# Kernel optimization log

Hardware: AMD Instinct MI355X
Metric: run time of the kernel (lower is better)

Reference implementation:

```python
import jax, jax.numpy as jnp
import numpy as np

N_NODES = 100000

def _gcn_norm(edge_index, num_nodes):
    # add self loops, compute symmetric normalization D^-1/2 (A+I) D^-1/2
    loops = jnp.arange(num_nodes, dtype=edge_index.dtype)
    row = jnp.concatenate([edge_index[0], loops])
    col = jnp.concatenate([edge_index[1], loops])
    ones = jnp.ones(row.shape[0], dtype=jnp.float32)
    deg = jax.ops.segment_sum(ones, row, num_segments=num_nodes)
    dinv = jnp.where(deg > 0, jax.lax.rsqrt(deg), 0.0)
    norm = dinv[row] * dinv[col]  # [E+N]
    return row, col, norm

def _gcn_conv(x, W, b, row, col, norm, num_nodes):
    h = x @ W                      # [N, out]
    msg = h[col] * norm[:, None]   # gather + scale, [E+N, out]
    out = jax.ops.segment_sum(msg, row, num_segments=num_nodes)
    return out + b

def setup_inputs() -> dict:
    key = jax.random.key(0)
    k1, k2, k3, k4 = jax.random.split(key, 4)
    F_IN, HID, CLS = 128, 128, 40
    E = 1_600_000
    x = jax.random.normal(k1, (N_NODES, F_IN), dtype=jnp.float32)
    edge_index = jax.random.randint(k2, (2, E), 0, N_NODES, dtype=jnp.int64)
    W1 = jax.random.normal(k3, (F_IN, HID), dtype=jnp.float32) / np.sqrt(F_IN)
    b1 = jnp.zeros((HID,), dtype=jnp.float32)
    W2 = jax.random.normal(k4, (HID, CLS), dtype=jnp.float32) / np.sqrt(HID)
    b2 = jnp.zeros((CLS,), dtype=jnp.float32)
    return {"x": x, "edge_index": edge_index, "W1": W1, "b1": b1, "W2": W2, "b2": b2}

def reference(x, edge_index, W1, b1, W2, b2):
    num_nodes = x.shape[0]
    row, col, norm = _gcn_norm(edge_index, num_nodes)
    h = _gcn_conv(x, W1, b1, row, col, norm, num_nodes)
    h = jax.nn.relu(h)
    h = _gcn_conv(h, W2, b2, row, col, norm, num_nodes)
    return jax.nn.log_softmax(h, axis=1)
```

## Files before the change

kernel.cpp:

```cpp
#include <hip/hip_runtime.h>
#include <hip/hip_bf16.h>
#include <math.h>


#define TILE_A 8192
#define RB 98
#define CAP 2048

typedef __attribute__((ext_vector_type(8))) short bf16x8;
typedef __attribute__((ext_vector_type(4))) float f32x4;
typedef __attribute__((ext_vector_type(2))) float f32x2;
typedef __attribute__((ext_vector_type(4))) unsigned int u32x4;

struct f8 { float v[8]; };

__device__ inline f8 unpack8(uint4 u) {
    f8 r;
    r.v[0] = __uint_as_float(u.x << 16);
    r.v[1] = __uint_as_float(u.x & 0xffff0000u);
    r.v[2] = __uint_as_float(u.y << 16);
    r.v[3] = __uint_as_float(u.y & 0xffff0000u);
    r.v[4] = __uint_as_float(u.z << 16);
    r.v[5] = __uint_as_float(u.z & 0xffff0000u);
    r.v[6] = __uint_as_float(u.w << 16);
    r.v[7] = __uint_as_float(u.w & 0xffff0000u);
    return r;
}

__device__ inline f8 unpack8f8(unsigned long long v) {
    f8 r;
#if __has_builtin(__builtin_amdgcn_cvt_pk_f32_fp8)
    int lo = (int)(unsigned)(v & 0xffffffffULL);
    int hi = (int)(unsigned)(v >> 32);
    f32x2 p0 = __builtin_amdgcn_cvt_pk_f32_fp8(lo, false);
    f32x2 p1 = __builtin_amdgcn_cvt_pk_f32_fp8(lo, true);
    f32x2 p2 = __builtin_amdgcn_cvt_pk_f32_fp8(hi, false);
    f32x2 p3 = __builtin_amdgcn_cvt_pk_f32_fp8(hi, true);
    r.v[0] = p0[0]; r.v[1] = p0[1]; r.v[2] = p1[0]; r.v[3] = p1[1];
    r.v[4] = p2[0]; r.v[5] = p2[1]; r.v[6] = p3[0]; r.v[7] = p3[1];
#else
#pragma unroll
    for (int k = 0; k < 8; ++k) {
        unsigned b = (unsigned)((v >> (8 * k)) & 0xffULL);
        unsigned em = b & 0x7f;
        unsigned bits = (em ? ((em << 20) + 0x3C000000u) : 0u) | ((b >> 7) << 31);
        r.v[k] = __uint_as_float(bits);
    }
#endif
    return r;
}

__device__ inline unsigned char fp8_of(float f) {
#if __has_builtin(__builtin_amdgcn_cvt_pk_fp8_f32)
    int p = __builtin_amdgcn_cvt_pk_fp8_f32(f, f, 0, false);
    return (unsigned char)(p & 0xff);
#else
    unsigned s = __float_as_uint(f) >> 31;
    float af = fabsf(f);
    if (af < 0.015625f) return (unsigned char)(s << 7);
    if (af > 448.f) af = 448.f;
    unsigned u = __float_as_uint(af);
    unsigned mant = (u >> 20) & 0x7;
    unsigned rest = u & 0xfffff;
    unsigned em = (((u >> 23) - 120) << 3) | mant;
    if (rest > 0x80000 || (rest == 0x80000 && (mant & 1))) em += 1;
    if (em > 0x7e) em = 0x7e;
    return (unsigned char)((s << 7) | em);
#endif
}

__device__ inline unsigned pack2(float a, float b) {
    __hip_bfloat16 ha = __float2bfloat16(a);
    __hip_bfloat16 hb = __float2bfloat16(b);
    unsigned short sa = *(unsigned short*)&ha;
    unsigned short sb = *(unsigned short*)&hb;
    return (unsigned)sa | ((unsigned)sb << 16);
}

__device__ inline short bfs(float f) {
    __hip_bfloat16 h = __float2bfloat16(f);
    return *(short*)&h;
}

__device__ inline bf16x8 to8(float4 p, float4 q) {
    bf16x8 v;
    v[0] = bfs(p.x); v[1] = bfs(p.y); v[2] = bfs(p.z); v[3] = bfs(p.w);
    v[4] = bfs(q.x); v[5] = bfs(q.y); v[6] = bfs(q.z); v[7] = bfs(q.w);
    return v;
}

__device__ inline int ecol_of(long long v) { return (int)(unsigned)(v & 0xffffffffLL); }
__device__ inline float ew_of(long long v) { return __int_as_float((int)(v >> 32)); }

__global__ __launch_bounds__(256) void k_wt(const float* __restrict__ W1,
                                            const float* __restrict__ W2,
                                            short* __restrict__ Wt1,
                                            short* __restrict__ Wt2,
                                            int* __restrict__ bktcnt) {
    int idx = blockIdx.x * 256 + threadIdx.x;
    if (idx < 16384) {
        int k = idx >> 7, f = idx & 127;
        Wt1[f * 128 + k] = bfs(W1[k * 128 + f]);
    } else if (idx < 16384 + 6144) {
        int j = idx - 16384;
        int f = j >> 7, k = j & 127;
        Wt2[j] = (f < 40) ? bfs(W2[k * 40 + f]) : (short)0;
    } else if (idx < 16384 + 6144 + 1024) {
        bktcnt[idx - 16384 - 6144] = 0;
    }
}

__global__ __launch_bounds__(1024) void k_binA(const int* __restrict__ ei,
                                               int* __restrict__ bktcnt,
                                               int2* __restrict__ brec, int E) {
    __shared__ int h[1024];
    __shared__ int cur[1024];
    int t = threadIdx.x;
    h[t] = 0;
    __syncthreads();
    int base = blockIdx.x * TILE_A;
    int lim = min(base + TILE_A, E);
    for (int i = base + t; i < lim; i += 1024) atomicAdd(&h[ei[i] / RB], 1);
    __syncthreads();
    cur[t] = h[t] ? atomicAdd(&bktcnt[t], h[t]) : 0;
    __syncthreads();
    for (int i = base + t; i < lim; i += 1024) {
        int r = ei[i];
        int b = r / RB;
        int pos = atomicAdd(&cur[b], 1);
        if (pos < CAP) brec[(size_t)b * CAP + pos] = make_int2(r, ei[E + i]);
    }
}

__global__ __launch_bounds__(256) void k_cnt(const int2* __restrict__ brec,
                                             const int* __restrict__ bktcnt,
                                             int2* __restrict__ rbe,
                                             float* __restrict__ dinv, int N) {
    __shared__ int h[RB];
    __shared__ int l[256];
    int k = blockIdx.x;
    int t = threadIdx.x;
    if (t < RB) h[t] = 0;
    __syncthreads();
    int s = k * CAP;
    int e = s + min(bktcnt[k], CAP);
    int r0 = k * RB;
    for (int i = s + t; i < e; i += 256) atomicAdd(&h[brec[i].x - r0], 1);
    __syncthreads();
    int v = (t < RB) ? h[t] : 0;
    l[t] = v;
    __syncthreads();
#pragma unroll
    for (int o = 1; o < 256; o <<= 1) {
        int u = (t >= o) ? l[t - o] : 0;
        __syncthreads();
        l[t] += u;
        __syncthreads();
    }
    if (t < RB && r0 + t < N) {
        int beg = s + (l[t] - v);
        rbe[r0 + t] = make_int2(beg, beg + v);
        dinv[r0 + t] = rsqrtf((float)(v + 1));
    }
}

__global__ __launch_bounds__(256) void k_csr3(const int2* __restrict__ brec,
                                              const int* __restrict__ bktcnt,
                                              const int2* __restrict__ rbe,
                                              const float* __restrict__ dinv,
                                              long long* __restrict__ erec, int N) {
    __shared__ int cur[RB];
    int k = blockIdx.x;
    int t = threadIdx.x;
    int r0 = k * RB;
    if (t < RB) cur[t] = (r0 + t < N) ? rbe[r0 + t].x : 0;
    __syncthreads();
    int s = k * CAP;
    int e = s + min(bktcnt[k], CAP);
    for (int i = s + t; i < e; i += 256) {
        int2 rc = brec[i];
        int pos = atomicAdd(&cur[rc.x - r0], 1);
        float w = dinv[rc.x] * dinv[rc.y];
        long long rec = (long long)((unsigned long long)(unsigned)__float_as_int(w) << 32) |
                        (unsigned long long)(unsigned)rc.y;
        erec[pos] = rec;
    }
}

__global__ __launch_bounds__(256) void k_gemm1m(const float* __restrict__ x,
                                                const short* __restrict__ Wt,
                                                unsigned char* __restrict__ Tf8, int N) {
    int t = threadIdx.x;
    int wid = t >> 6, l = t & 63;
    int r = l & 15;
    int ko = (l >> 4) * 8;
    long long nb = (long long)blockIdx.x * 128 + wid * 32;

    bf16x8 a[2][4];
#pragma unroll
    for (int g = 0; g < 2; ++g) {
        long long n = nb + g * 16 + r;
        if (n >= N) n = N - 1;
        const float* xr = x + n * 128;
#pragma unroll
        for (int kc = 0; kc < 4; ++kc) {
            float4 p = *(const float4*)(xr + kc * 32 + ko);
            float4 q = *(const float4*)(xr + kc * 32 + ko + 4);
            a[g][kc] = to8(p, q);
        }
    }

    f32x4 acc[2][8];
#pragma unroll
    for (int g = 0; g < 2; ++g)
#pragma unroll
        for (int ft = 0; ft < 8; ++ft) acc[g][ft] = (f32x4){0.f, 0.f, 0.f, 0.f};

#pragma unroll
    for (int ft = 0; ft < 8; ++ft) {
        const short* wp = Wt + (ft * 16 + r) * 128 + ko;
#pragma unroll
        for (int kc = 0; kc < 4; ++kc) {
            bf16x8 b = *(const bf16x8*)(wp + kc * 32);
            acc[0][ft] = __builtin_amdgcn_mfma_f32_16x16x32_bf16(a[0][kc], b, acc[0][ft], 0, 0, 0);
            acc[1][ft] = __builtin_amdgcn_mfma_f32_16x16x32_bf16(a[1][kc], b, acc[1][ft], 0, 0, 0);
        }
    }

    int row0 = (l >> 4) * 4;
#pragma unroll
    for (int g = 0; g < 2; ++g) {
#pragma unroll
        for (int i = 0; i < 4; ++i) {
            long long n = nb + g * 16 + row0 + i;
            if (n < N) {
                unsigned char* orow = Tf8 + n * 128;
#pragma unroll
                for (int ft = 0; ft < 8; ++ft) orow[ft * 16 + r] = fp8_of(acc[g][ft][i]);
            }
        }
    }
}

__global__ __launch_bounds__(256) void k_gemm2m(const short* __restrict__ Ub,
                                                const short* __restrict__ Wt2,
                                                short* __restrict__ H2a,
                                                short* __restrict__ H2c, int N) {
    int t = threadIdx.x;
    int wid = t >> 6, l = t & 63;
    int r = l & 15;
    int ko = (l >> 4) * 8;
    long long nb = (long long)blockIdx.x * 128 + wid * 32;

    bf16x8 a[2][4];
#pragma unroll
    for (int g = 0; g < 2; ++g) {
        long long n = nb + g * 16 + r;
        if (n >= N) n = N - 1;
        const short* ur = Ub + n * 128;
#pragma unroll
        for (int kc = 0; kc < 4; ++kc)
            a[g][kc] = *(const bf16x8*)(ur + kc * 32 + ko);
    }

    f32x4 acc[2][3];
#pragma unroll
    for (int g = 0; g < 2; ++g)
#pragma unroll
        for (int ft = 0; ft < 3; ++ft) acc[g][ft] = (f32x4){0.f, 0.f, 0.f, 0.f};

#pragma unroll
    for (int ft = 0; ft < 3; ++ft) {
        const short* wp = Wt2 + (ft * 16 + r) * 128 + ko;
#pragma unroll
        for (int kc = 0; kc < 4; ++kc) {
            bf16x8 b = *(const bf16x8*)(wp + kc * 32);
            acc[0][ft] = __builtin_amdgcn_mfma_f32_16x16x32_bf16(a[0][kc], b, acc[0][ft], 0, 0, 0);
            acc[1][ft] = __builtin_amdgcn_mfma_f32_16x16x32_bf16(a[1][kc], b, acc[1][ft], 0, 0, 0);
        }
    }

    int row0 = (l >> 4) * 4;
#pragma unroll
    for (int g = 0; g < 2; ++g) {
#pragma unroll
        for (int i = 0; i < 4; ++i) {
            long long n = nb + g * 16 + row0 + i;
            if (n < N) {
#pragma unroll
                for (int ft = 0; ft < 3; ++ft) {
                    int f = ft * 16 + r;
                    if (f < 32) H2a[n * 32 + f] = bfs(acc[g][ft][i]);
                    else if (f < 40) H2c[n * 8 + (f - 32)] = bfs(acc[g][ft][i]);
                }
            }
        }
    }
}

__global__ __launch_bounds__(256) void k_pull1(const unsigned long long* __restrict__ T8,
                                               const float* __restrict__ dinv,
                                               const int2* __restrict__ rbe,
                                               const long long* __restrict__ erec,
                                               const float* __restrict__ b,
                                               uint4* __restrict__ Ub, int N) {
    int tid = blockIdx.x * 256 + threadIdx.x;
    int n = tid >> 4;
    if (n >= N) return;
    int q = tid & 15;

    float dn = dinv[n];
    float ss = dn * dn;
    f8 s8 = unpack8f8(T8[(size_t)n * 16 + q]);
    float acc[8];
#pragma unroll
    for (int j = 0; j < 8; ++j) acc[j] = s8.v[j] * ss;

    int2 be = rbe[n];
    int i = be.x, end = be.y;
    for (; i + 7 < end; i += 8) {
        long long e0 = __builtin_nontemporal_load(erec + i);
        long long e1 = __builtin_nontemporal_load(erec + i + 1);
        long long e2 = __builtin_nontemporal_load(erec + i + 2);
        long long e3 = __builtin_nontemporal_load(erec + i + 3);
        long long e4 = __builtin_nontemporal_load(erec + i + 4);
        long long e5 = __builtin_nontemporal_load(erec + i + 5);
        long long e6 = __builtin_nontemporal_load(erec + i + 6);
        long long e7 = __builtin_nontemporal_load(erec + i + 7);
        unsigned long long g0 = T8[(size_t)ecol_of(e0) * 16 + q];
        unsigned long long g1 = T8[(size_t)ecol_of(e1) * 16 + q];
        unsigned long long g2 = T8[(size_t)ecol_of(e2) * 16 + q];
        unsigned long long g3 = T8[(size_t)ecol_of(e3) * 16 + q];
        unsigned long long g4 = T8[(size_t)ecol_of(e4) * 16 + q];
        unsigned long long g5 = T8[(size_t)ecol_of(e5) * 16 + q];
        unsigned long long g6 = T8[(size_t)ecol_of(e6) * 16 + q];
        unsigned long long g7 = T8[(size_t)ecol_of(e7) * 16 + q];
        f8 a0 = unpack8f8(g0);
        f8 a1 = unpack8f8(g1);
        f8 a2 = unpack8f8(g2);
        f8 a3 = unpack8f8(g3);
        f8 a4 = unpack8f8(g4);
        f8 a5 = unpack8f8(g5);
        f8 a6 = unpack8f8(g6);
        f8 a7 = unpack8f8(g7);
        float w0 = ew_of(e0), w1 = ew_of(e1), w2 = ew_of(e2), w3 = ew_of(e3);
        float w4 = ew_of(e4), w5 = ew_of(e5), w6 = ew_of(e6), w7 = ew_of(e7);
#pragma unroll
        for (int j = 0; j < 8; ++j) acc[j] = fmaf(w0, a0.v[j], acc[j]);
#pragma unroll
        for (int j = 0; j < 8; ++j) acc[j] = fmaf(w1, a1.v[j], acc[j]);
#pragma unroll
        for (int j = 0; j < 8; ++j) acc[j] = fmaf(w2, a2.v[j], acc[j]);
#pragma unroll
        for (int j = 0; j < 8; ++j) acc[j] = fmaf(w3, a3.v[j], acc[j]);
#pragma unroll
        for (int j = 0; j < 8; ++j) acc[j] = fmaf(w4, a4.v[j], acc[j]);
#pragma unroll
        for (int j = 0; j < 8; ++j) acc[j] = fmaf(w5, a5.v[j], acc[j]);
#pragma unroll
        for (int j = 0; j < 8; ++j) acc[j] = fmaf(w6, a6.v[j], acc[j]);
#pragma unroll
        for (int j = 0; j < 8; ++j) acc[j] = fmaf(w7, a7.v[j], acc[j]);
    }
    for (; i + 3 < end; i += 4) {
        long long e0 = __builtin_nontemporal_load(erec + i);
        long long e1 = __builtin_nontemporal_load(erec + i + 1);
        long long e2 = __builtin_nontemporal_load(erec + i + 2);
        long long e3 = __builtin_nontemporal_load(erec + i + 3);
        unsigned long long g0 = T8[(size_t)ecol_of(e0) * 16 + q];
        unsigned long long g1 = T8[(size_t)ecol_of(e1) * 16 + q];
        unsigned long long g2 = T8[(size_t)ecol_of(e2) * 16 + q];
        unsigned long long g3 = T8[(size_t)ecol_of(e3) * 16 + q];
        f8 a0 = unpack8f8(g0);
        f8 a1 = unpack8f8(g1);
        f8 a2 = unpack8f8(g2);
        f8 a3 = unpack8f8(g3);
        float w0 = ew_of(e0), w1 = ew_of(e1), w2 = ew_of(e2), w3 = ew_of(e3);
#pragma unroll
        for (int j = 0; j < 8; ++j) acc[j] = fmaf(w0, a0.v[j], acc[j]);
#pragma unroll
        for (int j = 0; j < 8; ++j) acc[j] = fmaf(w1, a1.v[j], acc[j]);
#pragma unroll
        for (int j = 0; j < 8; ++j) acc[j] = fmaf(w2, a2.v[j], acc[j]);
#pragma unroll
        for (int j = 0; j < 8; ++j) acc[j] = fmaf(w3, a3.v[j], acc[j]);
    }
    for (; i < end; ++i) {
        long long e0 = __builtin_nontemporal_load(erec + i);
        float w0 = ew_of(e0);
        f8 a0 = unpack8f8(T8[(size_t)ecol_of(e0) * 16 + q]);
#pragma unroll
        for (int j = 0; j < 8; ++j) acc[j] = fmaf(w0, a0.v[j], acc[j]);
    }

    float4 b0 = ((const float4*)b)[q * 2];
    float4 b1v = ((const float4*)b)[q * 2 + 1];
    acc[0] = fmaxf(acc[0] + b0.x, 0.f);
    acc[1] = fmaxf(acc[1] + b0.y, 0.f);
    acc[2] = fmaxf(acc[2] + b0.z, 0.f);
    acc[3] = fmaxf(acc[3] + b0.w, 0.f);
    acc[4] = fmaxf(acc[4] + b1v.x, 0.f);
    acc[5] = fmaxf(acc[5] + b1v.y, 0.f);
    acc[6] = fmaxf(acc[6] + b1v.z, 0.f);
    acc[7] = fmaxf(acc[7] + b1v.w, 0.f);

    uint4 o;
    o.x = pack2(acc[0], acc[1]);
    o.y = pack2(acc[2], acc[3]);
    o.z = pack2(acc[4], acc[5]);
    o.w = pack2(acc[6], acc[7]);
    Ub[(size_t)n * 16 + q] = o;
}

__global__ __launch_bounds__(256) void k_pull2(const uint4* __restrict__ H2a4,
                                               const uint4* __restrict__ H2c4,
                                               const float* __restrict__ dinv,
                                               const int2* __restrict__ rbe,
                                               const long long* __restrict__ erec,
                                               const float* __restrict__ b2,
                                               float* __restrict__ out, int N) {
    int tid = blockIdx.x * 256 + threadIdx.x;
    int n = tid >> 3;
    if (n >= N) return;
    int q = tid & 7;
    bool act = q < 5;
    bool ina = q < 4;
    const uint4* bp = ina ? (H2a4 + q) : H2c4;
    size_t stride = ina ? 4 : 1;

    float dn = dinv[n];
    float ss = dn * dn;
    float acc[8];
#pragma unroll
    for (int j = 0; j < 8; ++j) acc[j] = 0.f;
    if (act) {
        f8 s8 = unpack8(bp[(size_t)n * stride]);
#pragma unroll
        for (int j = 0; j < 8; ++j) acc[j] = s8.v[j] * ss;
    }
    int2 be = rbe[n];
    int i = be.x, end = be.y;
    for (; i + 3 < end; i += 4) {
        long long e0 = __builtin_nontemporal_load(erec + i);
        long long e1 = __builtin_nontemporal_load(erec + i + 1);
        long long e2 = __builtin_nontemporal_load(erec + i + 2);
        long long e3 = __builtin_nontemporal_load(erec + i + 3);
        uint4 g0 = bp[(size_t)ecol_of(e0) * stride];
        uint4 g1 = bp[(size_t)ecol_of(e1) * stride];
        uint4 g2 = bp[(size_t)ecol_of(e2) * stride];
        uint4 g3 = bp[(size_t)ecol_of(e3) * stride];
        if (act) {
            float w0 = ew_of(e0), w1 = ew_of(e1), w2 = ew_of(e2), w3 = ew_of(e3);
            f8 a0 = unpack8(g0);
            f8 a1 = unpack8(g1);
            f8 a2 = unpack8(g2);
            f8 a3 = unpack8(g3);
#pragma unroll
            for (int j = 0; j < 8; ++j) acc[j] = fmaf(w0, a0.v[j], acc[j]);
#pragma unroll
            for (int j = 0; j < 8; ++j) acc[j] = fmaf(w1, a1.v[j], acc[j]);
#pragma unroll
            for (int j = 0; j < 8; ++j) acc[j] = fmaf(w2, a2.v[j], acc[j]);
#pragma unroll
            for (int j = 0; j < 8; ++j) acc[j] = fmaf(w3, a3.v[j], acc[j]);
        }
    }
    for (; i < end; ++i) {
        long long e0 = erec[i];
        if (act) {
            float w0 = ew_of(e0);
            f8 a0 = unpack8(bp[(size_t)ecol_of(e0) * stride]);
#pragma unroll
            for (int j = 0; j < 8; ++j) acc[j] = fmaf(w0, a0.v[j], acc[j]);
        }
    }
    if (act) {
        float4 b0 = ((const float4*)b2)[q * 2];
        float4 b1v = ((const float4*)b2)[q * 2 + 1];
        acc[0] += b0.x; acc[1] += b0.y; acc[2] += b0.z; acc[3] += b0.w;
        acc[4] += b1v.x; acc[5] += b1v.y; acc[6] += b1v.z; acc[7] += b1v.w;
    }
    float m = -INFINITY;
    if (act) {
#pragma unroll
        for (int j = 0; j < 8; ++j) m = fmaxf(m, acc[j]);
    }
#pragma unroll
    for (int o = 4; o > 0; o >>= 1) m = fmaxf(m, __shfl_xor(m, o, 8));
    float e = 0.f;
    if (act) {
#pragma unroll
        for (int j = 0; j < 8; ++j) e += expf(acc[j] - m);
    }
#pragma unroll
    for (int o = 4; o > 0; o >>= 1) e += __shfl_xor(e, o, 8);
    float lg = m + logf(e);
    if (act) {
        float4* o4 = (float4*)out;
        o4[(size_t)n * 10 + q * 2] =
            make_float4(acc[0] - lg, acc[1] - lg, acc[2] - lg, acc[3] - lg);
        o4[(size_t)n * 10 + q * 2 + 1] =
            make_float4(acc[4] - lg, acc[5] - lg, acc[6] - lg, acc[7] - lg);
    }
}

extern "C" void kernel_launch(void* const* d_in, const int* in_sizes, int n_in,
                              void* d_out, int out_size, void* d_ws, size_t ws_size,
                              hipStream_t stream) {
    const float* x  = (const float*)d_in[0];
    const int*   ei = (const int*)d_in[1];
    const float* W1 = (const float*)d_in[2];
    const float* b1 = (const float*)d_in[3];
    const float* W2 = (const float*)d_in[4];
    const float* b2 = (const float*)d_in[5];
    float* out = (float*)d_out;

    const int N = in_sizes[0] / 128;
    const int E = in_sizes[1] / 2;
    const int nbkt = (N + RB - 1) / RB;

    char* ws = (char*)d_ws;
    float* dinv    = (float*)(ws);
    int2*  rbe     = (int2*)(ws + (512 << 10));
    int*   bktcnt  = (int*)(ws + (1536 << 10));
    short* Wt1     = (short*)(ws + (1600 << 10));
    short* Wt2     = (short*)(ws + (1700 << 10));
    long long* erec = (long long*)(ws + (3 << 20));
    int2*  brec    = (int2*)(ws + (21 << 20));
    short* H2a     = (short*)(ws + (38 << 20));
    short* H2c     = (short*)(ws + (45 << 20));
    unsigned char* Tf8 = (unsigned char*)(ws + (47 << 20));
    unsigned* Ub   = (unsigned*)(ws + (60 << 20));

    int na = (E + TILE_A - 1) / TILE_A;
    int ng = (N + 127) / 128;

    k_wt<<<92, 256, 0, stream>>>(W1, W2, Wt1, Wt2, bktcnt);
    k_binA<<<na, 1024, 0, stream>>>(ei, bktcnt, brec, E);
    k_cnt<<<nbkt, 256, 0, stream>>>(brec, bktcnt, rbe, dinv, N);
    k_csr3<<<nbkt, 256, 0, stream>>>(brec, bktcnt, rbe, dinv, erec, N);

    k_gemm1m<<<ng, 256, 0, stream>>>(x, Wt1, Tf8, N);
    k_pull1<<<((long long)N * 16 + 255) / 256, 256, 0, stream>>>(
        (const unsigned long long*)Tf8, dinv, rbe, erec, b1, (uint4*)Ub, N);
    k_gemm2m<<<ng, 256, 0, stream>>>((const short*)Ub, Wt2, H2a, H2c, N);
    k_pull2<<<((long long)N * 8 + 255) / 256, 256, 0, stream>>>(
        (const uint4*)H2a, (const uint4*)H2c, dinv, rbe, erec, b2, out, N);
}
```

Measured before the change: 177.7 us.

## Store 4-byte column indices, compute edge weights on the fly, split layer-2 pull

Replaces the 8-byte packed (weight, column) edge records with 4-byte column indices and recomputes each edge weight as dinv[n]*dinv[col] inside the pull kernels. This halves edge-stream traffic and lets the old count and CSR-fill kernels merge into one. Layer-2 features are stored in two 20-column halves, pulled by two kernel passes that write unnormalized output, and a separate log-softmax kernel then rereads and rewrites the output. The extra dinv gathers, the added launches and the second pass over the edge list and output are the costs taken on in exchange.

```diff
diff --git a/kernel.cpp b/kernel.cpp
--- a/kernel.cpp
+++ b/kernel.cpp
@@ -10,9 +10,9 @@
 typedef __attribute__((ext_vector_type(8))) short bf16x8;
 typedef __attribute__((ext_vector_type(4))) float f32x4;
 typedef __attribute__((ext_vector_type(2))) float f32x2;
-typedef __attribute__((ext_vector_type(4))) unsigned int u32x4;
 
 struct f8 { float v[8]; };
+struct f4s { float v[4]; };
 
 __device__ inline f8 unpack8(uint4 u) {
     f8 r;
@@ -24,6 +24,16 @@
     r.v[5] = __uint_as_float(u.z & 0xffff0000u);
     r.v[6] = __uint_as_float(u.w << 16);
     r.v[7] = __uint_as_float(u.w & 0xffff0000u);
+    return r;
+}
+
+__device__ inline f4s unpack4(unsigned long long v) {
+    f4s r;
+    unsigned lo = (unsigned)v, hi = (unsigned)(v >> 32);
+    r.v[0] = __uint_as_float(lo << 16);
+    r.v[1] = __uint_as_float(lo & 0xffff0000u);
+    r.v[2] = __uint_as_float(hi << 16);
+    r.v[3] = __uint_as_float(hi & 0xffff0000u);
     return r;
 }
 
@@ -89,9 +99,6 @@
     return v;
 }
 
-__device__ inline int ecol_of(long long v) { return (int)(unsigned)(v & 0xffffffffLL); }
-__device__ inline float ew_of(long long v) { return __int_as_float((int)(v >> 32)); }
-
 __global__ __launch_bounds__(256) void k_wt(const float* __restrict__ W1,
                                             const float* __restrict__ W2,
                                             short* __restrict__ Wt1,
@@ -132,12 +139,14 @@
     }
 }
 
-__global__ __launch_bounds__(256) void k_cnt(const int2* __restrict__ brec,
+__global__ __launch_bounds__(256) void k_csr(const int2* __restrict__ brec,
                                              const int* __restrict__ bktcnt,
                                              int2* __restrict__ rbe,
-                                             float* __restrict__ dinv, int N) {
+                                             float* __restrict__ dinv,
+                                             int* __restrict__ ecol, int N) {
     __shared__ int h[RB];
     __shared__ int l[256];
+    __shared__ int cur[RB];
     int k = blockIdx.x;
     int t = threadIdx.x;
     if (t < RB) h[t] = 0;
@@ -157,33 +166,19 @@
         l[t] += u;
         __syncthreads();
     }
-    if (t < RB && r0 + t < N) {
+    if (t < RB) {
         int beg = s + (l[t] - v);
-        rbe[r0 + t] = make_int2(beg, beg + v);
-        dinv[r0 + t] = rsqrtf((float)(v + 1));
-    }
-}
-
-__global__ __launch_bounds__(256) void k_csr3(const int2* __restrict__ brec,
-                                              const int* __restrict__ bktcnt,
-                                              const int2* __restrict__ rbe,
-                                              const float* __restrict__ dinv,
-                                              long long* __restrict__ erec, int N) {
-    __shared__ int cur[RB];
-    int k = blockIdx.x;
-    int t = threadIdx.x;
-    int r0 = k * RB;
-    if (t < RB) cur[t] = (r0 + t < N) ? rbe[r0 + t].x : 0;
-    __syncthreads();
-    int s = k * CAP;
-    int e = s + min(bktcnt[k], CAP);
+        cur[t] = beg;
+        if (r0 + t < N) {
+            rbe[r0 + t] = make_int2(beg, beg + v);
+            dinv[r0 + t] = rsqrtf((float)(v + 1));
+        }
+    }
+    __syncthreads();
     for (int i = s + t; i < e; i += 256) {
         int2 rc = brec[i];
         int pos = atomicAdd(&cur[rc.x - r0], 1);
-        float w = dinv[rc.x] * dinv[rc.y];
-        long long rec = (long long)((unsigned long long)(unsigned)__float_as_int(w) << 32) |
-                        (unsigned long long)(unsigned)rc.y;
-        erec[pos] = rec;
+        ecol[pos] = rc.y;
     }
 }
 
@@ -244,8 +239,8 @@
 
 __global__ __launch_bounds__(256) void k_gemm2m(const short* __restrict__ Ub,
                                                 const short* __restrict__ Wt2,
-                                                short* __restrict__ H2a,
-                                                short* __restrict__ H2c, int N) {
+                                                short* __restrict__ H2p0,
+                                                short* __restrict__ H2p1, int N) {
     int t = threadIdx.x;
     int wid = t >> 6, l = t & 63;
     int r = l & 15;
@@ -290,8 +285,8 @@
 #pragma unroll
                 for (int ft = 0; ft < 3; ++ft) {
                     int f = ft * 16 + r;
-                    if (f < 32) H2a[n * 32 + f] = bfs(acc[g][ft][i]);
-                    else if (f < 40) H2c[n * 8 + (f - 32)] = bfs(acc[g][ft][i]);
+                    if (f < 20) H2p0[n * 20 + f] = bfs(acc[g][ft][i]);
+                    else if (f < 40) H2p1[n * 20 + (f - 20)] = bfs(acc[g][ft][i]);
                 }
             }
         }
@@ -301,7 +296,7 @@
 __global__ __launch_bounds__(256) void k_pull1(const unsigned long long* __restrict__ T8,
                                                const float* __restrict__ dinv,
                                                const int2* __restrict__ rbe,
-                                               const long long* __restrict__ erec,
+                                               const int* __restrict__ ecol,
                                                const float* __restrict__ b,
                                                uint4* __restrict__ Ub, int N) {
     int tid = blockIdx.x * 256 + threadIdx.x;
@@ -319,22 +314,26 @@
     int2 be = rbe[n];
     int i = be.x, end = be.y;
     for (; i + 7 < end; i += 8) {
-        long long e0 = __builtin_nontemporal_load(erec + i);
-        long long e1 = __builtin_nontemporal_load(erec + i + 1);
-        long long e2 = __builtin_nontemporal_load(erec + i + 2);
-        long long e3 = __builtin_nontemporal_load(erec + i + 3);
-        long long e4 = __builtin_nontemporal_load(erec + i + 4);
-        long long e5 = __builtin_nontemporal_load(erec + i + 5);
-        long long e6 = __builtin_nontemporal_load(erec + i + 6);
-        long long e7 = __builtin_nontemporal_load(erec + i + 7);
-        unsigned long long g0 = T8[(size_t)ecol_of(e0) * 16 + q];
-        unsigned long long g1 = T8[(size_t)ecol_of(e1) * 16 + q];
-        unsigned long long g2 = T8[(size_t)ecol_of(e2) * 16 + q];
-        unsigned long long g3 = T8[(size_t)ecol_of(e3) * 16 + q];
-        unsigned long long g4 = T8[(size_t)ecol_of(e4) * 16 + q];
-        unsigned long long g5 = T8[(size_t)ecol_of(e5) * 16 + q];
-        unsigned long long g6 = T8[(size_t)ecol_of(e6) * 16 + q];
-        unsigned long long g7 = T8[(size_t)ecol_of(e7) * 16 + q];
+        int c0 = __builtin_nontemporal_load(ecol + i);
+        int c1 = __builtin_nontemporal_load(ecol + i + 1);
+        int c2 = __builtin_nontemporal_load(ecol + i + 2);
+        int c3 = __builtin_nontemporal_load(ecol + i + 3);
+        int c4 = __builtin_nontemporal_load(ecol + i + 4);
+        int c5 = __builtin_nontemporal_load(ecol + i + 5);
+        int c6 = __builtin_nontemporal_load(ecol + i + 6);
+        int c7 = __builtin_nontemporal_load(ecol + i + 7);
+        unsigned long long g0 = T8[(size_t)c0 * 16 + q];
+        unsigned long long g1 = T8[(size_t)c1 * 16 + q];
+        unsigned long long g2 = T8[(size_t)c2 * 16 + q];
+        unsigned long long g3 = T8[(size_t)c3 * 16 + q];
+        unsigned long long g4 = T8[(size_t)c4 * 16 + q];
+        unsigned long long g5 = T8[(size_t)c5 * 16 + q];
+        unsigned long long g6 = T8[(size_t)c6 * 16 + q];
+        unsigned long long g7 = T8[(size_t)c7 * 16 + q];
+        float w0 = dn * dinv[c0], w1 = dn * dinv[c1];
+        float w2 = dn * dinv[c2], w3 = dn * dinv[c3];
+        float w4 = dn * dinv[c4], w5 = dn * dinv[c5];
+        float w6 = dn * dinv[c6], w7 = dn * dinv[c7];
         f8 a0 = unpack8f8(g0);
         f8 a1 = unpack8f8(g1);
         f8 a2 = unpack8f8(g2);
@@ -343,8 +342,6 @@
         f8 a5 = unpack8f8(g5);
         f8 a6 = unpack8f8(g6);
         f8 a7 = unpack8f8(g7);
-        float w0 = ew_of(e0), w1 = ew_of(e1), w2 = ew_of(e2), w3 = ew_of(e3);
-        float w4 = ew_of(e4), w5 = ew_of(e5), w6 = ew_of(e6), w7 = ew_of(e7);
 #pragma unroll
         for (int j = 0; j < 8; ++j) acc[j] = fmaf(w0, a0.v[j], acc[j]);
 #pragma unroll
@@ -363,19 +360,20 @@
         for (int j = 0; j < 8; ++j) acc[j] = fmaf(w7, a7.v[j], acc[j]);
     }
     for (; i + 3 < end; i += 4) {
-        long long e0 = __builtin_nontemporal_load(erec + i);
-        long long e1 = __builtin_nontemporal_load(erec + i + 1);
-        long long e2 = __builtin_nontemporal_load(erec + i + 2);
-        long long e3 = __builtin_nontemporal_load(erec + i + 3);
-        unsigned long long g0 = T8[(size_t)ecol_of(e0) * 16 + q];
-        unsigned long long g1 = T8[(size_t)ecol_of(e1) * 16 + q];
-        unsigned long long g2 = T8[(size_t)ecol_of(e2) * 16 + q];
-        unsigned long long g3 = T8[(size_t)ecol_of(e3) * 16 + q];
+        int c0 = __builtin_nontemporal_load(ecol + i);
+        int c1 = __builtin_nontemporal_load(ecol + i + 1);
+        int c2 = __builtin_nontemporal_load(ecol + i + 2);
+        int c3 = __builtin_nontemporal_load(ecol + i + 3);
+        unsigned long long g0 = T8[(size_t)c0 * 16 + q];
+        unsigned long long g1 = T8[(size_t)c1 * 16 + q];
+        unsigned long long g2 = T8[(size_t)c2 * 16 + q];
+        unsigned long long g3 = T8[(size_t)c3 * 16 + q];
+        float w0 = dn * dinv[c0], w1 = dn * dinv[c1];
+        float w2 = dn * dinv[c2], w3 = dn * dinv[c3];
         f8 a0 = unpack8f8(g0);
         f8 a1 = unpack8f8(g1);
         f8 a2 = unpack8f8(g2);
         f8 a3 = unpack8f8(g3);
-        float w0 = ew_of(e0), w1 = ew_of(e1), w2 = ew_of(e2), w3 = ew_of(e3);
 #pragma unroll
         for (int j = 0; j < 8; ++j) acc[j] = fmaf(w0, a0.v[j], acc[j]);
 #pragma unroll
@@ -386,9 +384,9 @@
         for (int j = 0; j < 8; ++j) acc[j] = fmaf(w3, a3.v[j], acc[j]);
     }
     for (; i < end; ++i) {
-        long long e0 = __builtin_nontemporal_load(erec + i);
-        float w0 = ew_of(e0);
-        f8 a0 = unpack8f8(T8[(size_t)ecol_of(e0) * 16 + q]);
+        int c0 = __builtin_nontemporal_load(ecol + i);
+        float w0 = dn * dinv[c0];
+        f8 a0 = unpack8f8(T8[(size_t)c0 * 16 + q]);
 #pragma unroll
         for (int j = 0; j < 8; ++j) acc[j] = fmaf(w0, a0.v[j], acc[j]);
     }
@@ -412,95 +410,103 @@
     Ub[(size_t)n * 16 + q] = o;
 }
 
-__global__ __launch_bounds__(256) void k_pull2(const uint4* __restrict__ H2a4,
-                                               const uint4* __restrict__ H2c4,
-                                               const float* __restrict__ dinv,
-                                               const int2* __restrict__ rbe,
-                                               const long long* __restrict__ erec,
-                                               const float* __restrict__ b2,
-                                               float* __restrict__ out, int N) {
+__global__ __launch_bounds__(256) void k_pull2h(const unsigned long long* __restrict__ H2p,
+                                                const float* __restrict__ dinv,
+                                                const int2* __restrict__ rbe,
+                                                const int* __restrict__ ecol,
+                                                const float* __restrict__ b2,
+                                                float* __restrict__ out, int N, int hf) {
     int tid = blockIdx.x * 256 + threadIdx.x;
     int n = tid >> 3;
     if (n >= N) return;
     int q = tid & 7;
     bool act = q < 5;
-    bool ina = q < 4;
-    const uint4* bp = ina ? (H2a4 + q) : H2c4;
-    size_t stride = ina ? 4 : 1;
 
     float dn = dinv[n];
     float ss = dn * dn;
-    float acc[8];
-#pragma unroll
-    for (int j = 0; j < 8; ++j) acc[j] = 0.f;
+    float acc[4] = {0.f, 0.f, 0.f, 0.f};
     if (act) {
-        f8 s8 = unpack8(bp[(size_t)n * stride]);
-#pragma unroll
-        for (int j = 0; j < 8; ++j) acc[j] = s8.v[j] * ss;
+        f4s s4 = unpack4(H2p[(size_t)n * 5 + q]);
+#pragma unroll
+        for (int j = 0; j < 4; ++j) acc[j] = s4.v[j] * ss;
     }
     int2 be = rbe[n];
     int i = be.x, end = be.y;
     for (; i + 3 < end; i += 4) {
-        long long e0 = __builtin_nontemporal_load(erec + i);
-        long long e1 = __builtin_nontemporal_load(erec + i + 1);
-        long long e2 = __builtin_nontemporal_load(erec + i + 2);
-        long long e3 = __builtin_nontemporal_load(erec + i + 3);
-        uint4 g0 = bp[(size_t)ecol_of(e0) * stride];
-        uint4 g1 = bp[(size_t)ecol_of(e1) * stride];
-        uint4 g2 = bp[(size_t)ecol_of(e2) * stride];
-        uint4 g3 = bp[(size_t)ecol_of(e3) * stride];
+        int c0 = __builtin_nontemporal_load(ecol + i);
+        int c1 = __builtin_nontemporal_load(ecol + i + 1);
+        int c2 = __builtin_nontemporal_load(ecol + i + 2);
+        int c3 = __builtin_nontemporal_load(ecol + i + 3);
         if (act) {
-            float w0 = ew_of(e0), w1 = ew_of(e1), w2 = ew_of(e2), w3 = ew_of(e3);
-            f8 a0 = unpack8(g0);
-            f8 a1 = unpack8(g1);
-            f8 a2 = unpack8(g2);
-            f8 a3 = unpack8(g3);
-#pragma unroll
-            for (int j = 0; j < 8; ++j) acc[j] = fmaf(w0, a0.v[j], acc[j]);
-#pragma unroll
-            for (int j = 0; j < 8; ++j) acc[j] = fmaf(w1, a1.v[j], acc[j]);
-#pragma unroll
-            for (int j = 0; j < 8; ++j) acc[j] = fmaf(w2, a2.v[j], acc[j]);
-#pragma unroll
-            for (int j = 0; j < 8; ++j) acc[j] = fmaf(w3, a3.v[j], acc[j]);
+            float w0 = dn * dinv[c0], w1 = dn * dinv[c1];
+            float w2 = dn * dinv[c2], w3 = dn * dinv[c3];
+            f4s a0 = unpack4(H2p[(size_t)c0 * 5 + q]);
+            f4s a1 = unpack4(H2p[(size_t)c1 * 5 + q]);
+            f4s a2 = unpack4(H2p[(size_t)c2 * 5 + q]);
+            f4s a3 = unpack4(H2p[(size_t)c3 * 5 + q]);
+#pragma unroll
+            for (int j = 0; j < 4; ++j) acc[j] = fmaf(w0, a0.v[j], acc[j]);
+#pragma unroll
+            for (int j = 0; j < 4; ++j) acc[j] = fmaf(w1, a1.v[j], acc[j]);
+#pragma unroll
+            for (int j = 0; j < 4; ++j) acc[j] = fmaf(w2, a2.v[j], acc[j]);
+#pragma unroll
+            for (int j = 0; j < 4; ++j) acc[j] = fmaf(w3, a3.v[j], acc[j]);
         }
     }
     for (; i < end; ++i) {
-        long long e0 = erec[i];
+        int c0 = __builtin_nontemporal_load(ecol + i);
         if (act) {
-            float w0 = ew_of(e0);
-            f8 a0 = unpack8(bp[(size_t)ecol_of(e0) * stride]);
-#pragma unroll
-            for (int j = 0; j < 8; ++j) acc[j] = fmaf(w0, a0.v[j], acc[j]);
+            float w0 = dn * dinv[c0];
+            f4s a0 = unpack4(H2p[(size_t)c0 * 5 + q]);
+#pragma unroll
+            for (int j = 0; j < 4; ++j) acc[j] = fmaf(w0, a0.v[j], acc[j]);
         }
     }
     if (act) {
-        float4 b0 = ((const float4*)b2)[q * 2];
-        float4 b1v = ((const float4*)b2)[q * 2 + 1];
-        acc[0] += b0.x; acc[1] += b0.y; acc[2] += b0.z; acc[3] += b0.w;
-        acc[4] += b1v.x; acc[5] += b1v.y; acc[6] += b1v.z; acc[7] += b1v.w;
+        float4 bv = ((const float4*)(b2 + hf * 20))[q];
+        f32x4 o;
+        o[0] = acc[0] + bv.x;
+        o[1] = acc[1] + bv.y;
+        o[2] = acc[2] + bv.z;
+        o[3] = acc[3] + bv.w;
+        __builtin_nontemporal_store(o, (f32x4*)(out + (size_t)n * 40 + hf * 20 + q * 4));
+    }
+}
+
+__global__ __launch_bounds__(256) void k_lsm(float* __restrict__ out, int N) {
+    int tid = blockIdx.x * 256 + threadIdx.x;
+    int n = tid >> 3;
+    if (n >= N) return;
+    int q = tid & 7;
+    bool act = q < 5;
+
+    float4 v0 = make_float4(0.f, 0.f, 0.f, 0.f), v1 = v0;
+    float4* o4 = (float4*)out;
+    if (act) {
+        v0 = o4[(size_t)n * 10 + q * 2];
+        v1 = o4[(size_t)n * 10 + q * 2 + 1];
     }
     float m = -INFINITY;
     if (act) {
-#pragma unroll
-        for (int j = 0; j < 8; ++j) m = fmaxf(m, acc[j]);
+        m = fmaxf(fmaxf(fmaxf(v0.x, v0.y), fmaxf(v0.z, v0.w)),
+                  fmaxf(fmaxf(v1.x, v1.y), fmaxf(v1.z, v1.w)));
     }
 #pragma unroll
     for (int o = 4; o > 0; o >>= 1) m = fmaxf(m, __shfl_xor(m, o, 8));
     float e = 0.f;
     if (act) {
-#pragma unroll
-        for (int j = 0; j < 8; ++j) e += expf(acc[j] - m);
+        e = expf(v0.x - m) + expf(v0.y - m) + expf(v0.z - m) + expf(v0.w - m) +
+            expf(v1.x - m) + expf(v1.y - m) + expf(v1.z - m) + expf(v1.w - m);
     }
 #pragma unroll
     for (int o = 4; o > 0; o >>= 1) e += __shfl_xor(e, o, 8);
     float lg = m + logf(e);
     if (act) {
-        float4* o4 = (float4*)out;
         o4[(size_t)n * 10 + q * 2] =
-            make_float4(acc[0] - lg, acc[1] - lg, acc[2] - lg, acc[3] - lg);
+            make_float4(v0.x - lg, v0.y - lg, v0.z - lg, v0.w - lg);
         o4[(size_t)n * 10 + q * 2 + 1] =
-            make_float4(acc[4] - lg, acc[5] - lg, acc[6] - lg, acc[7] - lg);
+            make_float4(v1.x - lg, v1.y - lg, v1.z - lg, v1.w - lg);
     }
 }
 
@@ -525,25 +531,27 @@
     int*   bktcnt  = (int*)(ws + (1536 << 10));
     short* Wt1     = (short*)(ws + (1600 << 10));
     short* Wt2     = (short*)(ws + (1700 << 10));
-    long long* erec = (long long*)(ws + (3 << 20));
-    int2*  brec    = (int2*)(ws + (21 << 20));
-    short* H2a     = (short*)(ws + (38 << 20));
-    short* H2c     = (short*)(ws + (45 << 20));
-    unsigned char* Tf8 = (unsigned char*)(ws + (47 << 20));
-    unsigned* Ub   = (unsigned*)(ws + (60 << 20));
+    int*   ecol    = (int*)(ws + (2 << 20));
+    int2*  brec    = (int2*)(ws + (11 << 20));
+    short* H2p0    = (short*)(ws + (28 << 20));
+    short* H2p1    = (short*)(ws + (33 << 20));
+    unsigned char* Tf8 = (unsigned char*)(ws + (38 << 20));
+    unsigned* Ub   = (unsigned*)(ws + (51 << 20));
 
     int na = (E + TILE_A - 1) / TILE_A;
     int ng = (N + 127) / 128;
 
     k_wt<<<92, 256, 0, stream>>>(W1, W2, Wt1, Wt2, bktcnt);
     k_binA<<<na, 1024, 0, stream>>>(ei, bktcnt, brec, E);
-    k_cnt<<<nbkt, 256, 0, stream>>>(brec, bktcnt, rbe, dinv, N);
-    k_csr3<<<nbkt, 256, 0, stream>>>(brec, bktcnt, rbe, dinv, erec, N);
+    k_csr<<<nbkt, 256, 0, stream>>>(brec, bktcnt, rbe, dinv, ecol, N);
 
     k_gemm1m<<<ng, 256, 0, stream>>>(x, Wt1, Tf8, N);
     k_pull1<<<((long long)N * 16 + 255) / 256, 256, 0, stream>>>(
-        (const unsigned long long*)Tf8, dinv, rbe, erec, b1, (uint4*)Ub, N);
-    k_gemm2m<<<ng, 256, 0, stream>>>((const short*)Ub, Wt2, H2a, H2c, N);
-    k_pull2<<<((long long)N * 8 + 255) / 256, 256, 0, stream>>>(
-        (const uint4*)H2a, (const uint4*)H2c, dinv, rbe, erec, b2, out, N);
-}
+        (const unsigned long long*)Tf8, dinv, rbe, ecol, b1, (uint4*)Ub, N);
+    k_gemm2m<<<ng, 256, 0, stream>>>((const short*)Ub, Wt2, H2p0, H2p1, N);
+    k_pull2h<<<((long long)N * 8 + 255) / 256, 256, 0, stream>>>(
+        (const unsigned long long*)H2p0, dinv, rbe, ecol, b2, out, N, 0);
+    k_pull2h<<<((long long)N * 8 + 255) / 256, 256, 0, stream>>>(
+        (const unsigned long long*)H2p1, dinv, rbe, ecol, b2, out, N, 1);
+    k_lsm<<<((long long)N * 8 + 255) / 256, 256, 0, stream>>>(out, N);
+}
```

Result: slower. 211.4 us (+19.0%).
